# Kernel optimization log

Hardware: AMD Instinct MI355X
Metric: run time of the kernel (lower is better)

The kernel has to match this reference:

```python
import jax, jax.numpy as jnp
import numpy as np

_EPS = 1e-12      # degenerate-triangle denominator guard
_CHUNK = 64       # triangles processed per scan step


def _bary(p, a, b, c):
    """Barycentric coords of points p w.r.t. triangle (a,b,c). Broadcasts.
    Returns [..., 3] = (u, v, w); -1 everywhere for degenerate triangles."""
    v0 = b - a
    v1 = c - a
    v2 = p - a
    d00 = jnp.sum(v0 * v0, -1)
    d01 = jnp.sum(v0 * v1, -1)
    d11 = jnp.sum(v1 * v1, -1)
    d20 = jnp.sum(v2 * v0, -1)
    d21 = jnp.sum(v2 * v1, -1)
    denom = d00 * d11 - d01 * d01
    bad = jnp.abs(denom) < _EPS
    ds = jnp.where(bad, 1.0, denom)
    v = (d11 * d20 - d01 * d21) / ds
    w = (d00 * d21 - d01 * d20) / ds
    u = 1.0 - v - w
    bar = jnp.stack([u, v, w], -1)
    return jnp.where(bad[..., None], -1.0, bar)


def _pixel_grid(res):
    # pixel-center UVs; x = u along columns, y = v along rows
    t = (jnp.arange(res, dtype=jnp.float32) + 0.5) / res
    gy, gx = jnp.meshgrid(t, t, indexing='ij')
    return jnp.stack([gx, gy], -1)  # [res, res, 2]


def _rasterize_ids(uv, face_indices, res):
    """For each bake pixel, the index of the first (lowest-index) triangle
    containing it, or -1 (== rast[...,-1] in the slang kernel)."""
    px = _pixel_grid(res)                    # [H, W, 2]
    tri = uv[face_indices]                   # [Nf, 3, 2]
    nf = tri.shape[0]
    nchunk = nf // _CHUNK
    tri_c = tri[: nchunk * _CHUNK].reshape(nchunk, _CHUNK, 3, 2)
    fid0 = jnp.full((res, res), -1, dtype=jnp.int32)

    def step(fid, xs):
        ci, tc = xs                          # tc: [C, 3, 2]
        bar = _bary(px[:, :, None, :], tc[:, 0], tc[:, 1], tc[:, 2])  # [H, W, C, 3]
        inside = jnp.all(bar >= 0.0, axis=-1)                          # [H, W, C]
        hit = jnp.any(inside, axis=-1)
        first = jnp.argmax(inside, axis=-1).astype(jnp.int32)          # first hit in chunk
        cand = ci * _CHUNK + first
        fid = jnp.where(hit & (fid < 0), cand, fid)
        return fid, None

    fid, _ = jax.lax.scan(step, fid0, (jnp.arange(nchunk, dtype=jnp.int32), tri_c))
    return fid


def _interpolate(attr, uv, face_indices, fid, res):
    px = _pixel_grid(res)
    tri_idx = face_indices[jnp.clip(fid, 0)]        # [H, W, 3] vertex ids of hit face
    verts = uv[tri_idx]                             # [H, W, 3, 2]
    bar = _bary(px, verts[..., 0, :], verts[..., 1, :], verts[..., 2, :])  # [H, W, 3]
    av = attr[tri_idx]                              # [H, W, 3, 3]
    out = jnp.einsum('hwk,hwkc->hwc', bar, av)
    return jnp.where(fid[..., None] >= 0, out, 0.0)  # zeros outside coverage (kernel inits output to 0)


def setup_inputs() -> dict:
    key = jax.random.key(0)
    k1, k2, k3 = jax.random.split(key, 3)
    Nv, Nf, res = 50000, 512, 512
    attr = jax.random.normal(k1, (Nv, 3), dtype=jnp.float32)
    uv = jax.random.uniform(k2, (Nv, 2), dtype=jnp.float32)
    face_indices = jax.random.randint(k3, (Nf, 3), 0, Nv, dtype=jnp.int32)
    return {"attr": attr, "uv": uv, "face_indices": face_indices, "bake_resolution": res}


def reference(attr, uv, face_indices, bake_resolution):
    fid = _rasterize_ids(uv, face_indices, bake_resolution)
    return _interpolate(attr, uv, face_indices, fid, bake_resolution)
```

## Files before the change

kernel.cpp:

```cpp
#include <hip/hip_runtime.h>
#include <math.h>

#pragma clang fp contract(off)

#define TB_NT 512
#define TS 16

__device__ inline int lanes_below(unsigned long long m) {
    return __builtin_amdgcn_mbcnt_hi((unsigned int)(m >> 32),
           __builtin_amdgcn_mbcnt_lo((unsigned int)m, 0u));
}

__global__ void tb_setup(const float* __restrict__ uv,
                         const int*   __restrict__ fidx,
                         float4* __restrict__ R0, float4* __restrict__ R1,
                         float2* __restrict__ R2, float4* __restrict__ BB,
                         int n_used) {
    int t = blockIdx.x * blockDim.x + threadIdx.x;
    if (t >= n_used) return;
    int i0 = fidx[3 * t + 0];
    int i1 = fidx[3 * t + 1];
    int i2 = fidx[3 * t + 2];
    float ax = uv[2 * i0], ay = uv[2 * i0 + 1];
    float bx = uv[2 * i1], by = uv[2 * i1 + 1];
    float cx = uv[2 * i2], cy = uv[2 * i2 + 1];
    float v0x = bx - ax, v0y = by - ay;
    float v1x = cx - ax, v1y = cy - ay;
    float d00 = v0x * v0x + v0y * v0y;
    float d01 = v0x * v1x + v0y * v1y;
    float d11 = v1x * v1x + v1y * v1y;
    float denom = d00 * d11 - d01 * d01;
    float ds = (fabsf(denom) < 1e-12f) ? 0.0f : denom;
    R0[t] = make_float4(ax, ay, v0x, v0y);
    R1[t] = make_float4(v1x, v1y, d01, ds);
    R2[t] = make_float2(d11, d00);
    if (ds == 0.0f) {
        BB[t] = make_float4(2.0f, -1.0f, 2.0f, -1.0f);
    } else {
        BB[t] = make_float4(fminf(ax, fminf(bx, cx)),
                            fmaxf(ax, fmaxf(bx, cx)),
                            fminf(ay, fminf(by, cy)),
                            fmaxf(ay, fmaxf(by, cy)));
    }
}

__global__ __launch_bounds__(256)
void tb_bake(const float*  __restrict__ attr,
             const int*    __restrict__ fidx,
             const float4* __restrict__ R0, const float4* __restrict__ R1,
             const float4* __restrict__ R2q, const float4* __restrict__ BB,
             float* __restrict__ out,
             int res, int n_used, int tiles_x) {
    __shared__ float4 sA[TB_NT];
    __shared__ float4 sB[TB_NT];
    __shared__ float2 sC[TB_NT];
    __shared__ float4 sBB[TB_NT];
    __shared__ unsigned short sList[4][TB_NT + 1];

    int bx = blockIdx.x % tiles_x;
    int by = blockIdx.x / tiles_x;
    int tx = threadIdx.x & (TS - 1);
    int ty = threadIdx.x >> 4;
    int w = bx * TS + tx;
    int h = by * TS + ty;
    bool live = (w < res) && (h < res);
    int pix = h * res + w;
    float pxx = ((float)w + 0.5f) / (float)res;
    float pxy = ((float)h + 0.5f) / (float)res;

    int wv = threadIdx.x >> 6;
    int ln = threadIdx.x & 63;

    float wx0 = (float)(bx * TS) / (float)res;
    float wx1 = (float)(bx * TS + TS) / (float)res;
    float wy0 = (float)(by * TS + wv * 4) / (float)res;
    float wy1 = (float)(by * TS + wv * 4 + 4) / (float)res;

    for (int i = threadIdx.x; i < n_used; i += 256) {
        sA[i]  = R0[i];
        sB[i]  = R1[i];
        sBB[i] = BB[i];
    }
    {
        float4* sC4 = (float4*)sC;
        int n4 = n_used >> 1;
        for (int i = threadIdx.x; i < n4; i += 256) sC4[i] = R2q[i];
    }
    __syncthreads();

    int cnt = 0;
    for (int r = 0; r * 64 < n_used; ++r) {
        int t = r * 64 + ln;
        bool p = false;
        if (t < n_used) {
            float4 bb = sBB[t];
            p = (bb.y >= wx0) && (bb.x <= wx1) && (bb.w >= wy0) && (bb.z <= wy1);
        }
        unsigned long long m = __ballot((int)p);
        if (p) sList[wv][cnt + lanes_below(m)] = (unsigned short)t;
        cnt += __popcll(m);
    }
    if (ln == 0) sList[wv][cnt] = 0;

    int   hit = -1;
    float bu = 0.0f, bv = 0.0f, bw = 0.0f;

    if (live && cnt > 0) {
        int t = sList[wv][0];
        float4 qa = sA[t];
        float4 qb = sB[t];
        float2 qc = sC[t];
        for (int i = 0; i < cnt; ++i) {
            int tn = sList[wv][i + 1];
            float4 qan = sA[tn];
            float4 qbn = sB[tn];
            float2 qcn = sC[tn];
            float v2x = pxx - qa.x;
            float v2y = pxy - qa.y;
            float d20 = v2x * qa.z + v2y * qa.w;
            float d21 = v2x * qb.x + v2y * qb.y;
            float vn = qc.x * d20 - qb.z * d21;
            float wn = qc.y * d21 - qb.z * d20;
            float ds = qb.w;
            float sg = (ds > 0.0f) ? 1.0f : -1.0f;
            if (hit < 0 && vn * sg >= 0.0f && wn * sg >= 0.0f) {
                float v  = vn / ds;
                float ww = wn / ds;
                float u  = (1.0f - v) - ww;
                if (u >= 0.0f) {
                    bu = u; bv = v; bw = ww;
                    hit = t;
                }
            }
            if (__all((int)(hit >= 0))) break;
            qa = qan; qb = qbn; qc = qcn; t = tn;
        }
    }

    if (live) {
        float o0 = 0.0f, o1 = 0.0f, o2 = 0.0f;
        if (hit >= 0) {
            int i0 = fidx[3 * hit + 0];
            int i1 = fidx[3 * hit + 1];
            int i2 = fidx[3 * hit + 2];
            o0 = (bu * attr[3 * i0 + 0] + bv * attr[3 * i1 + 0]) + bw * attr[3 * i2 + 0];
            o1 = (bu * attr[3 * i0 + 1] + bv * attr[3 * i1 + 1]) + bw * attr[3 * i2 + 1];
            o2 = (bu * attr[3 * i0 + 2] + bv * attr[3 * i1 + 2]) + bw * attr[3 * i2 + 2];
        }
        out[3 * pix + 0] = o0;
        out[3 * pix + 1] = o1;
        out[3 * pix + 2] = o2;
    }
}

extern "C" void kernel_launch(void* const* d_in, const int* in_sizes, int n_in,
                              void* d_out, int out_size, void* d_ws, size_t ws_size,
                              hipStream_t stream) {
    const float* attr = (const float*)d_in[0];
    const float* uv   = (const float*)d_in[1];
    const int*   fidx = (const int*)d_in[2];
    float*       out  = (float*)d_out;

    int res = (int)lround(sqrt((double)(out_size / 3)));
    int nf = in_sizes[2] / 3;
    int n_used = (nf / 64) * 64;

    float4* R0 = (float4*)d_ws;
    float4* R1 = R0 + TB_NT;
    float2* R2 = (float2*)(R1 + TB_NT);
    float4* BB = (float4*)(R2 + TB_NT);

    if (n_used > 0) {
        tb_setup<<<(n_used + 255) / 256, 256, 0, stream>>>(uv, fidx, R0, R1, R2, BB, n_used);
    }
    int tiles_x = (res + TS - 1) / TS;
    int nblocks = tiles_x * tiles_x;
    tb_bake<<<nblocks, 256, 0, stream>>>(attr, fidx, R0, R1, (const float4*)R2, BB,
                                         out, res, n_used, tiles_x);
}
```

Before: 79.44 us.

## Stream triangles per-wave in slabs with compacted shared buffers, drop block sync

Each wave stops waiting for the whole block to stage all triangle data into shared memory. It now reads triangle records from global memory in slabs of 192, culls them by bounding box, and writes only the surviving records into a per-wave shared buffer. The intent is to remove the block-wide __syncthreads, cut the shared-memory footprint for better occupancy, and let waves that are already fully hit stop fetching early. In exchange, each wave issues its own global loads for all candidate triangles, so the same data is read redundantly across waves, and it no longer prefetches the next triangle during the test loop.

```diff
diff --git a/kernel.cpp b/kernel.cpp
--- a/kernel.cpp
+++ b/kernel.cpp
@@ -3,8 +3,9 @@
 
 #pragma clang fp contract(off)
 
-#define TB_NT 512
-#define TS 16
+#define TB_NT   512
+#define TB_SLAB 192
+#define TS      16
 
 __device__ inline int lanes_below(unsigned long long m) {
     return __builtin_amdgcn_mbcnt_hi((unsigned int)(m >> 32),
@@ -48,14 +49,13 @@
 void tb_bake(const float*  __restrict__ attr,
              const int*    __restrict__ fidx,
              const float4* __restrict__ R0, const float4* __restrict__ R1,
-             const float4* __restrict__ R2q, const float4* __restrict__ BB,
+             const float2* __restrict__ R2, const float4* __restrict__ BB,
              float* __restrict__ out,
              int res, int n_used, int tiles_x) {
-    __shared__ float4 sA[TB_NT];
-    __shared__ float4 sB[TB_NT];
-    __shared__ float2 sC[TB_NT];
-    __shared__ float4 sBB[TB_NT];
-    __shared__ unsigned short sList[4][TB_NT + 1];
+    __shared__ float4         sR0[4][TB_SLAB];
+    __shared__ float4         sR1[4][TB_SLAB];
+    __shared__ float2         sR2[4][TB_SLAB];
+    __shared__ unsigned short sId[4][TB_SLAB];
 
     int bx = blockIdx.x % tiles_x;
     int by = blockIdx.x / tiles_x;
@@ -76,45 +76,37 @@
     float wy0 = (float)(by * TS + wv * 4) / (float)res;
     float wy1 = (float)(by * TS + wv * 4 + 4) / (float)res;
 
-    for (int i = threadIdx.x; i < n_used; i += 256) {
-        sA[i]  = R0[i];
-        sB[i]  = R1[i];
-        sBB[i] = BB[i];
-    }
-    {
-        float4* sC4 = (float4*)sC;
-        int n4 = n_used >> 1;
-        for (int i = threadIdx.x; i < n4; i += 256) sC4[i] = R2q[i];
-    }
-    __syncthreads();
-
-    int cnt = 0;
-    for (int r = 0; r * 64 < n_used; ++r) {
-        int t = r * 64 + ln;
-        bool p = false;
-        if (t < n_used) {
-            float4 bb = sBB[t];
-            p = (bb.y >= wx0) && (bb.x <= wx1) && (bb.w >= wy0) && (bb.z <= wy1);
-        }
-        unsigned long long m = __ballot((int)p);
-        if (p) sList[wv][cnt + lanes_below(m)] = (unsigned short)t;
-        cnt += __popcll(m);
-    }
-    if (ln == 0) sList[wv][cnt] = 0;
-
     int   hit = -1;
     float bu = 0.0f, bv = 0.0f, bw = 0.0f;
 
-    if (live && cnt > 0) {
-        int t = sList[wv][0];
-        float4 qa = sA[t];
-        float4 qb = sB[t];
-        float2 qc = sC[t];
+    for (int base = 0; base < n_used; base += TB_SLAB) {
+        if (__all((int)(hit >= 0))) break;
+        int nb = min(TB_SLAB, n_used - base);
+
+        int cnt = 0;
+        for (int r = 0; r * 64 < nb; ++r) {
+            int t = base + r * 64 + ln;
+            float4 bb = BB[t];
+            float4 r0 = R0[t];
+            float4 r1 = R1[t];
+            float2 r2 = R2[t];
+            bool p = (bb.y >= wx0) && (bb.x <= wx1) &&
+                     (bb.w >= wy0) && (bb.z <= wy1);
+            unsigned long long m = __ballot((int)p);
+            if (p) {
+                int idx = cnt + lanes_below(m);
+                sR0[wv][idx] = r0;
+                sR1[wv][idx] = r1;
+                sR2[wv][idx] = r2;
+                sId[wv][idx] = (unsigned short)t;
+            }
+            cnt += __popcll(m);
+        }
+
         for (int i = 0; i < cnt; ++i) {
-            int tn = sList[wv][i + 1];
-            float4 qan = sA[tn];
-            float4 qbn = sB[tn];
-            float2 qcn = sC[tn];
+            float4 qa = sR0[wv][i];
+            float4 qb = sR1[wv][i];
+            float2 qc = sR2[wv][i];
             float v2x = pxx - qa.x;
             float v2y = pxy - qa.y;
             float d20 = v2x * qa.z + v2y * qa.w;
@@ -129,11 +121,10 @@
                 float u  = (1.0f - v) - ww;
                 if (u >= 0.0f) {
                     bu = u; bv = v; bw = ww;
-                    hit = t;
+                    hit = (int)sId[wv][i];
                 }
             }
             if (__all((int)(hit >= 0))) break;
-            qa = qan; qb = qbn; qc = qcn; t = tn;
         }
     }
 
@@ -175,6 +166,6 @@
     }
     int tiles_x = (res + TS - 1) / TS;
     int nblocks = tiles_x * tiles_x;
-    tb_bake<<<nblocks, 256, 0, stream>>>(attr, fidx, R0, R1, (const float4*)R2, BB,
+    tb_bake<<<nblocks, 256, 0, stream>>>(attr, fidx, R0, R1, R2, BB,
                                          out, res, n_used, tiles_x);
 }
```

Measured after the change: 80.15 us. Within noise of the previous version (+0.9%).
